# Kernel optimization log

Hardware: AMD Instinct MI355X
Metric: run time of the kernel (lower is better)

## Reference

```python
import jax, jax.numpy as jnp
import numpy as np
from jax import lax

C = 64      # mid_channels
CR = 16     # reduced channels (C // reduction_ratio 4)
G = 4       # groups (C // group_channels 16)
K = 7       # involution kernel size
L = 6       # number of involution layers (n_layers - 2)
EPS = 1e-5
DN = ('NCHW', 'OIHW', 'NCHW')


def conv3(x, w, b):
    # 3x3 conv, stride 1, no padding (torch Conv2d default)
    y = lax.conv_general_dilated(x, w, (1, 1), [(0, 0), (0, 0)], dimension_numbers=DN)
    return y + b[None, :, None, None]


def conv1x1(x, w, b):
    # pointwise conv as einsum over channels
    return jnp.einsum('oi,bihw->bohw', w, x) + b[None, :, None, None]


def involution(x, wr, br, g, bt, mu, var, ws, bs):
    B, Cc, H, W = x.shape
    # kernel generation: 1x1 reduce -> BN (eval) -> ReLU -> 1x1 span
    t = conv1x1(x, wr, br)
    t = (t - mu[None, :, None, None]) * (g * jax.lax.rsqrt(var + EPS))[None, :, None, None] + bt[None, :, None, None]
    t = jax.nn.relu(t)
    w = conv1x1(t, ws, bs)                    # (B, G*K*K, H, W)
    w = w.reshape(B, G, K * K, H, W)
    # unfold: patches ordered (C, Kh, Kw) along channel dim, matching torch unfold
    p = lax.conv_general_dilated_patches(x, (K, K), (1, 1), [(K // 2, K // 2)] * 2, dimension_numbers=DN)
    p = p.reshape(B, G, Cc // G, K * K, H, W)
    out = jnp.einsum('bgkhw,bgckhw->bgchw', w, p)
    return out.reshape(B, Cc, H, W)


def setup_inputs() -> dict:
    key = jax.random.key(0)
    ks = jax.random.split(key, 9)
    s = 0.05
    return {
        'input_tensor': jax.random.normal(ks[0], (1, 3, 128, 128), jnp.float32),
        'conv_in_w': jax.random.normal(ks[1], (C, 3, 3, 3), jnp.float32) * s,
        'conv_in_b': jax.random.normal(ks[2], (C,), jnp.float32) * s,
        'w_reduce': jax.random.normal(ks[3], (L, CR, C), jnp.float32) * s,
        'b_reduce': jax.random.normal(ks[4], (L, CR), jnp.float32) * s,
        'bn_gamma': jnp.ones((L, CR), jnp.float32),
        'bn_beta': jnp.zeros((L, CR), jnp.float32),
        'bn_mean': jnp.zeros((L, CR), jnp.float32),
        'bn_var': jnp.ones((L, CR), jnp.float32),
        'w_span': jax.random.normal(ks[5], (L, G * K * K, CR), jnp.float32) * s,
        'b_span': jax.random.normal(ks[6], (L, G * K * K), jnp.float32) * s,
        'conv_out_w': jax.random.normal(ks[7], (2 * C, C, 3, 3), jnp.float32) * s,
        'conv_out_b': jax.random.normal(ks[8], (2 * C,), jnp.float32) * s,
    }


def reference(input_tensor, conv_in_w, conv_in_b, w_reduce, b_reduce, bn_gamma,
              bn_beta, bn_mean, bn_var, w_span, b_span, conv_out_w, conv_out_b):
    x = conv3(input_tensor, conv_in_w, conv_in_b)          # (1, 64, 126, 126)
    for i in range(L):
        x = jax.nn.relu(involution(x, w_reduce[i], b_reduce[i], bn_gamma[i],
                                   bn_beta[i], bn_mean[i], bn_var[i],
                                   w_span[i], b_span[i]))
    return conv3(x, conv_out_w, conv_out_b)                # (1, 128, 124, 124)
```

## Files before the change

kernel.cpp:

```cpp
#include <hip/hip_runtime.h>

#define IH 126
#define IW 126
#define HW 15876
#define OH 124
#define OW 124
#define OHW 15376

__global__ __launch_bounds__(256) void conv_in_kernel(
    const float* __restrict__ x, const float* __restrict__ w,
    const float* __restrict__ b, float* __restrict__ y)
{
  int pix = blockIdx.x * 256 + threadIdx.x;
  if (pix >= HW) return;
  int oc = blockIdx.y;
  int h  = pix / IW;
  int wc = pix - h * IW;
  const float* wp = w + oc * 27;
  float acc = b[oc];
#pragma unroll
  for (int ci = 0; ci < 3; ci++)
#pragma unroll
    for (int ky = 0; ky < 3; ky++)
#pragma unroll
      for (int kx = 0; kx < 3; kx++)
        acc = fmaf(x[ci * 128 * 128 + (h + ky) * 128 + (wc + kx)],
                   wp[ci * 9 + ky * 3 + kx], acc);
  y[oc * HW + pix] = acc;
}

#define XSW(c, pos) ((c) ^ (((pos) & 7) << 3))
#define WVP 36
__global__ __launch_bounds__(512, 4) void inv_kernel(
    const float* __restrict__ x, float* __restrict__ y,
    const float* __restrict__ wr, const float* __restrict__ br,
    const float* __restrict__ gam, const float* __restrict__ bet,
    const float* __restrict__ mu, const float* __restrict__ var,
    const float* __restrict__ wspan, const float* __restrict__ bspan)
{
  __shared__ __align__(16) float xs[140][68];
  __shared__ __align__(16) float wvs[196 * WVP];
  __shared__ __align__(16) float tss[640];
  float* ob  = &xs[0][0];

  int tid = threadIdx.x;
  int bx = blockIdx.x & 15, by = blockIdx.x >> 4;
  int ox0 = bx * 8, oy0 = by * 4;
  int xh0 = ox0 - 3, yh0 = oy0 - 3;

  for (int idx = tid; idx < 140 * 64; idx += 512) {
    int c = idx / 140;
    int pos = idx - c * 140;
    int row = pos / 14;
    int col = pos - row * 14;
    int gy = yh0 + row, gx = xh0 + col;
    float v = 0.f;
    if (gy >= 0 && gy < IH && gx >= 0 && gx < IW)
      v = x[c * HW + gy * IW + gx];
    xs[pos][XSW(c, pos)] = v;
  }
  __syncthreads();

  int w_ = __builtin_amdgcn_readfirstlane(tid >> 6);
  int ln = tid & 63;
  int p  = ln & 31;
  int prow = p >> 3, pcol = p & 7;
  int pc = (prow + 3) * 14 + (pcol + 3);

  {
    int cr0 = 2 * w_;
    const float* wa = wr + cr0 * 64;
    const float* wb = wa + 64;
    float a0 = 0.f, a1 = 0.f;
    int xsw = (pc & 7) << 3;
#pragma unroll
    for (int ci = 0; ci < 64; ci += 4) {
      int cis = ci ^ xsw;
      float4 xv = *(const float4*)&xs[pc][cis];
      a0 = fmaf(xv.x, wa[cis + 0], a0); a1 = fmaf(xv.x, wb[cis + 0], a1);
      a0 = fmaf(xv.y, wa[cis + 1], a0); a1 = fmaf(xv.y, wb[cis + 1], a1);
      a0 = fmaf(xv.z, wa[cis + 2], a0); a1 = fmaf(xv.z, wb[cis + 2], a1);
      a0 = fmaf(xv.w, wa[cis + 3], a0); a1 = fmaf(xv.w, wb[cis + 3], a1);
    }
    float s0 = gam[cr0]     * rsqrtf(var[cr0]     + 1e-5f);
    float s1 = gam[cr0 + 1] * rsqrtf(var[cr0 + 1] + 1e-5f);
    float t0 = (a0 + br[cr0]     - mu[cr0])     * s0 + bet[cr0];
    float t1 = (a1 + br[cr0 + 1] - mu[cr0 + 1]) * s1 + bet[cr0 + 1];
    if (ln < 32) {
      tss[p * 20 + cr0]     = fmaxf(t0, 0.f);
      tss[p * 20 + cr0 + 1] = fmaxf(t1, 0.f);
    }
  }
  __syncthreads();

  {
    float tv[16];
#pragma unroll
    for (int i = 0; i < 4; i++) {
      float4 t4 = *(const float4*)&tss[p * 20 + 4 * i];
      tv[4 * i] = t4.x; tv[4 * i + 1] = t4.y;
      tv[4 * i + 2] = t4.z; tv[4 * i + 3] = t4.w;
    }
    for (int j = 0; j < 25; j++) {
      int pair = w_ + 8 * j;
      if (pair < 196) {
        const float* wk = wspan + pair * 16;
        float a = bspan[pair];
#pragma unroll
        for (int i = 0; i < 16; i++) a = fmaf(tv[i], wk[i], a);
        if (ln < 32) wvs[pair * WVP + pcol * 4 + prow] = a;
      }
    }
  }
  __syncthreads();

  float acc0 = 0.f, acc1 = 0.f, acc2 = 0.f, acc3 = 0.f;
  {
    int c = ln;
    int g = ln >> 4;
    float xw[4][7];
#pragma unroll
    for (int r = 0; r < 4; r++)
#pragma unroll
      for (int kx = 0; kx < 7; kx++) {
        int pos = r * 14 + w_ + kx;
        xw[r][kx] = xs[pos][XSW(c, pos)];
      }
#pragma unroll
    for (int ky = 0; ky < 7; ky++) {
      if (ky > 0) {
#pragma unroll
        for (int r = 0; r < 3; r++)
#pragma unroll
          for (int kx = 0; kx < 7; kx++) xw[r][kx] = xw[r + 1][kx];
#pragma unroll
        for (int kx = 0; kx < 7; kx++) {
          int pos = (ky + 3) * 14 + w_ + kx;
          xw[3][kx] = xs[pos][XSW(c, pos)];
        }
      }
#pragma unroll
      for (int kx = 0; kx < 7; kx++) {
        int k = ky * 7 + kx;
        float4 w4 = *(const float4*)&wvs[(g * 49 + k) * WVP + w_ * 4];
        acc0 = fmaf(w4.x, xw[0][kx], acc0);
        acc1 = fmaf(w4.y, xw[1][kx], acc1);
        acc2 = fmaf(w4.z, xw[2][kx], acc2);
        acc3 = fmaf(w4.w, xw[3][kx], acc3);
      }
    }
  }
  __syncthreads();

  {
    int c = ln;
    ob[c * 33 + 0 * 8 + w_] = fmaxf(acc0, 0.f);
    ob[c * 33 + 1 * 8 + w_] = fmaxf(acc1, 0.f);
    ob[c * 33 + 2 * 8 + w_] = fmaxf(acc2, 0.f);
    ob[c * 33 + 3 * 8 + w_] = fmaxf(acc3, 0.f);
  }
  __syncthreads();
  for (int j = tid; j < 2048; j += 512) {
    int c2 = j >> 5, pp = j & 31;
    int pr = pp >> 3, pc2 = pp & 7;
    int gy = oy0 + pr, gx = ox0 + pc2;
    if (gy < IH && gx < IW)
      y[c2 * HW + gy * IW + gx] = ob[c2 * 33 + pp];
  }
}

__global__ __launch_bounds__(256) void transpose_w_kernel(
    const float* __restrict__ w, float* __restrict__ wt)
{
  int i = blockIdx.x * 256 + threadIdx.x;
  if (i >= 128 * 64 * 9) return;
  int oc = i / 576;
  int rem = i - oc * 576;
  int ci = rem / 9;
  int k = rem - ci * 9;
  wt[(k * 64 + ci) * 128 + oc] = w[i];
}

__global__ __launch_bounds__(256, 6) void conv_out_kernel(
    const float* __restrict__ x, const float* __restrict__ wt,
    const float* __restrict__ b, float* __restrict__ y)
{
  __shared__ __align__(16) float xsm[16 * 100 * 4];
  int tid = threadIdx.x;
  int bx = blockIdx.x & 15, by = blockIdx.x >> 4;
  int oy0 = by * 8, ox0 = bx * 8;

  for (int u = tid; u < 1600; u += 256) {
    int cq = u / 100;
    int pos = u - cq * 100;
    int row = pos / 10;
    int col = pos - row * 10;
    int gy = oy0 + row, gx = ox0 + col;
    float4 v = make_float4(0.f, 0.f, 0.f, 0.f);
    if (gy < IH && gx < IW) {
      const float* xp = x + cq * 4 * HW + gy * IW + gx;
      v.x = xp[0]; v.y = xp[HW]; v.z = xp[2 * HW]; v.w = xp[3 * HW];
    }
    *(float4*)&xsm[u * 4] = v;
  }
  __syncthreads();

  int ln = tid & 63;
  int px = ln & 7, py = ln >> 3;
  int wv_ = __builtin_amdgcn_readfirstlane(tid >> 6);
  int oc8 = blockIdx.y * 32 + wv_ * 8;

  float acc[8];
#pragma unroll
  for (int j = 0; j < 8; j++) acc[j] = b[oc8 + j];

#pragma unroll
  for (int ky = 0; ky < 3; ky++) {
#pragma unroll
    for (int kx = 0; kx < 3; kx++) {
      int k = ky * 3 + kx;
      int pidx = (py + ky) * 10 + px + kx;
      const float* wp = wt + k * 64 * 128 + oc8;
#pragma unroll 4
      for (int cq = 0; cq < 16; cq++) {
        float4 xv = *(const float4*)&xsm[(cq * 100 + pidx) * 4];
        const float* wq = wp + cq * 4 * 128;
#pragma unroll
        for (int j = 0; j < 8; j++) {
          acc[j] = fmaf(xv.x, wq[0 * 128 + j], acc[j]);
          acc[j] = fmaf(xv.y, wq[1 * 128 + j], acc[j]);
          acc[j] = fmaf(xv.z, wq[2 * 128 + j], acc[j]);
          acc[j] = fmaf(xv.w, wq[3 * 128 + j], acc[j]);
        }
      }
    }
  }

  int oy = oy0 + py, ox = ox0 + px;
  if (oy < OH && ox < OW) {
#pragma unroll
    for (int j = 0; j < 8; j++)
      y[(oc8 + j) * OHW + oy * OW + ox] = acc[j];
  }
}

extern "C" void kernel_launch(void* const* d_in, const int* in_sizes, int n_in,
                              void* d_out, int out_size, void* d_ws, size_t ws_size,
                              hipStream_t stream)
{
  const float* input = (const float*)d_in[0];
  const float* ciw   = (const float*)d_in[1];
  const float* cib   = (const float*)d_in[2];
  const float* wred  = (const float*)d_in[3];
  const float* bred  = (const float*)d_in[4];
  const float* gam   = (const float*)d_in[5];
  const float* bet   = (const float*)d_in[6];
  const float* mu    = (const float*)d_in[7];
  const float* var   = (const float*)d_in[8];
  const float* wspan = (const float*)d_in[9];
  const float* bspan = (const float*)d_in[10];
  const float* cow   = (const float*)d_in[11];
  const float* cob   = (const float*)d_in[12];
  float* out = (float*)d_out;

  float* bufA = (float*)d_ws;
  float* bufB = bufA + (1 << 20);
  float* wt   = bufA + (1 << 21);

  transpose_w_kernel<<<288, 256, 0, stream>>>(cow, wt);
  conv_in_kernel<<<dim3(63, 64), 256, 0, stream>>>(input, ciw, cib, bufA);

  float* cur = bufA; float* nxt = bufB;
  for (int i = 0; i < 6; i++) {
    inv_kernel<<<512, 512, 0, stream>>>(cur, nxt,
        wred + i * 16 * 64, bred + i * 16, gam + i * 16, bet + i * 16,
        mu + i * 16, var + i * 16, wspan + i * 196 * 16, bspan + i * 196);
    float* t = cur; cur = nxt; nxt = t;
  }
  conv_out_kernel<<<dim3(256, 4), 256, 0, stream>>>(cur, wt, cob, out);
}
```

Before: 263.2 us.

## Fuse six involution layers into one cooperative kernel with grid sync

```diff
diff --git a/kernel.cpp b/kernel.cpp
--- a/kernel.cpp
+++ b/kernel.cpp
@@ -1,4 +1,7 @@
 #include <hip/hip_runtime.h>
+#include <hip/hip_cooperative_groups.h>
+
+namespace cg = cooperative_groups;
 
 #define IH 126
 #define IW 126
@@ -31,6 +34,163 @@
 
 #define XSW(c, pos) ((c) ^ (((pos) & 7) << 3))
 #define WVP 36
+
+__global__ __launch_bounds__(512, 4) void inv_all_kernel(
+    float* __restrict__ bufA, float* __restrict__ bufB,
+    const float* __restrict__ wr0, const float* __restrict__ br0,
+    const float* __restrict__ gam0, const float* __restrict__ bet0,
+    const float* __restrict__ mu0, const float* __restrict__ var0,
+    const float* __restrict__ wspan0, const float* __restrict__ bspan0)
+{
+  __shared__ __align__(16) float xs[140][68];
+  __shared__ __align__(16) float wvs[196 * WVP];
+  __shared__ __align__(16) float tss[640];
+  __shared__ __align__(16) float wsm[3136];
+  float* ob = &xs[0][0];
+
+  cg::grid_group grid = cg::this_grid();
+
+  int tid = threadIdx.x;
+  int bx = blockIdx.x & 15, by = blockIdx.x >> 4;
+  int ox0 = bx * 8, oy0 = by * 4;
+  int xh0 = ox0 - 3, yh0 = oy0 - 3;
+  int w_ = __builtin_amdgcn_readfirstlane(tid >> 6);
+  int ln = tid & 63;
+  int p  = ln & 31;
+  int prow = p >> 3, pcol = p & 7;
+  int pc = (prow + 3) * 14 + (pcol + 3);
+
+  for (int layer = 0; layer < 6; layer++) {
+    if (layer > 0) grid.sync();
+
+    const float* x     = (layer & 1) ? bufB : bufA;
+    float*       y     = (layer & 1) ? bufA : bufB;
+    const float* wr    = wr0    + layer * 16 * 64;
+    const float* br    = br0    + layer * 16;
+    const float* gam   = gam0   + layer * 16;
+    const float* bet   = bet0   + layer * 16;
+    const float* mu    = mu0    + layer * 16;
+    const float* var   = var0   + layer * 16;
+    const float* wspan = wspan0 + layer * 196 * 16;
+    const float* bspan = bspan0 + layer * 196;
+
+    for (int idx = tid; idx < 140 * 64; idx += 512) {
+      int c = idx / 140;
+      int pos = idx - c * 140;
+      int row = pos / 14;
+      int col = pos - row * 14;
+      int gy = yh0 + row, gx = xh0 + col;
+      float v = 0.f;
+      if (gy >= 0 && gy < IH && gx >= 0 && gx < IW)
+        v = x[c * HW + gy * IW + gx];
+      xs[pos][XSW(c, pos)] = v;
+    }
+    for (int j = tid; j < 3136; j += 512) wsm[j] = wspan[j];
+    __syncthreads();
+
+    {
+      int cr0 = 2 * w_;
+      const float* wa = wr + cr0 * 64;
+      const float* wb = wa + 64;
+      float a0 = 0.f, a1 = 0.f;
+      int xsw = (pc & 7) << 3;
+#pragma unroll
+      for (int ci = 0; ci < 64; ci += 4) {
+        int cis = ci ^ xsw;
+        float4 xv = *(const float4*)&xs[pc][cis];
+        a0 = fmaf(xv.x, wa[cis + 0], a0); a1 = fmaf(xv.x, wb[cis + 0], a1);
+        a0 = fmaf(xv.y, wa[cis + 1], a0); a1 = fmaf(xv.y, wb[cis + 1], a1);
+        a0 = fmaf(xv.z, wa[cis + 2], a0); a1 = fmaf(xv.z, wb[cis + 2], a1);
+        a0 = fmaf(xv.w, wa[cis + 3], a0); a1 = fmaf(xv.w, wb[cis + 3], a1);
+      }
+      float s0 = gam[cr0]     * rsqrtf(var[cr0]     + 1e-5f);
+      float s1 = gam[cr0 + 1] * rsqrtf(var[cr0 + 1] + 1e-5f);
+      float t0 = (a0 + br[cr0]     - mu[cr0])     * s0 + bet[cr0];
+      float t1 = (a1 + br[cr0 + 1] - mu[cr0 + 1]) * s1 + bet[cr0 + 1];
+      if (ln < 32) {
+        tss[p * 20 + cr0]     = fmaxf(t0, 0.f);
+        tss[p * 20 + cr0 + 1] = fmaxf(t1, 0.f);
+      }
+    }
+    __syncthreads();
+
+    {
+      float tv[16];
+#pragma unroll
+      for (int i = 0; i < 4; i++) {
+        float4 t4 = *(const float4*)&tss[p * 20 + 4 * i];
+        tv[4 * i] = t4.x; tv[4 * i + 1] = t4.y;
+        tv[4 * i + 2] = t4.z; tv[4 * i + 3] = t4.w;
+      }
+      for (int j = 0; j < 25; j++) {
+        int pair = w_ + 8 * j;
+        if (pair < 196) {
+          const float* wk = &wsm[pair * 16];
+          float a = bspan[pair];
+#pragma unroll
+          for (int i = 0; i < 16; i++) a = fmaf(tv[i], wk[i], a);
+          if (ln < 32) wvs[pair * WVP + pcol * 4 + prow] = a;
+        }
+      }
+    }
+    __syncthreads();
+
+    float acc0 = 0.f, acc1 = 0.f, acc2 = 0.f, acc3 = 0.f;
+    {
+      int c = ln;
+      int g = ln >> 4;
+      float xw[4][7];
+#pragma unroll
+      for (int r = 0; r < 4; r++)
+#pragma unroll
+        for (int kx = 0; kx < 7; kx++) {
+          int pos = r * 14 + w_ + kx;
+          xw[r][kx] = xs[pos][XSW(c, pos)];
+        }
+#pragma unroll
+      for (int ky = 0; ky < 7; ky++) {
+        if (ky > 0) {
+#pragma unroll
+          for (int r = 0; r < 3; r++)
+#pragma unroll
+            for (int kx = 0; kx < 7; kx++) xw[r][kx] = xw[r + 1][kx];
+#pragma unroll
+          for (int kx = 0; kx < 7; kx++) {
+            int pos = (ky + 3) * 14 + w_ + kx;
+            xw[3][kx] = xs[pos][XSW(c, pos)];
+          }
+        }
+#pragma unroll
+        for (int kx = 0; kx < 7; kx++) {
+          int k = ky * 7 + kx;
+          float4 w4 = *(const float4*)&wvs[(g * 49 + k) * WVP + w_ * 4];
+          acc0 = fmaf(w4.x, xw[0][kx], acc0);
+          acc1 = fmaf(w4.y, xw[1][kx], acc1);
+          acc2 = fmaf(w4.z, xw[2][kx], acc2);
+          acc3 = fmaf(w4.w, xw[3][kx], acc3);
+        }
+      }
+    }
+    __syncthreads();
+
+    {
+      int c = ln;
+      ob[c * 33 + 0 * 8 + w_] = fmaxf(acc0, 0.f);
+      ob[c * 33 + 1 * 8 + w_] = fmaxf(acc1, 0.f);
+      ob[c * 33 + 2 * 8 + w_] = fmaxf(acc2, 0.f);
+      ob[c * 33 + 3 * 8 + w_] = fmaxf(acc3, 0.f);
+    }
+    __syncthreads();
+    for (int j = tid; j < 2048; j += 512) {
+      int c2 = j >> 5, pp = j & 31;
+      int pr = pp >> 3, pc2 = pp & 7;
+      int gy = oy0 + pr, gx = ox0 + pc2;
+      if (gy < IH && gx < IW)
+        y[c2 * HW + gy * IW + gx] = ob[c2 * 33 + pp];
+    }
+  }
+}
+
 __global__ __launch_bounds__(512, 4) void inv_kernel(
     const float* __restrict__ x, float* __restrict__ y,
     const float* __restrict__ wr, const float* __restrict__ br,
@@ -270,12 +430,23 @@
   transpose_w_kernel<<<288, 256, 0, stream>>>(cow, wt);
   conv_in_kernel<<<dim3(63, 64), 256, 0, stream>>>(input, ciw, cib, bufA);
 
-  float* cur = bufA; float* nxt = bufB;
-  for (int i = 0; i < 6; i++) {
-    inv_kernel<<<512, 512, 0, stream>>>(cur, nxt,
-        wred + i * 16 * 64, bred + i * 16, gam + i * 16, bet + i * 16,
-        mu + i * 16, var + i * 16, wspan + i * 196 * 16, bspan + i * 196);
-    float* t = cur; cur = nxt; nxt = t;
-  }
-  conv_out_kernel<<<dim3(256, 4), 256, 0, stream>>>(cur, wt, cob, out);
-}
+  {
+    void* args[] = {&bufA, &bufB, (void*)&wred, (void*)&bred, (void*)&gam,
+                    (void*)&bet, (void*)&mu, (void*)&var, (void*)&wspan,
+                    (void*)&bspan};
+    hipError_t e = hipLaunchCooperativeKernel(
+        reinterpret_cast<void*>(inv_all_kernel), dim3(512), dim3(512),
+        args, 0, stream);
+    if (e != hipSuccess) {
+      float* cur = bufA; float* nxt = bufB;
+      for (int i = 0; i < 6; i++) {
+        inv_kernel<<<512, 512, 0, stream>>>(cur, nxt,
+            wred + i * 16 * 64, bred + i * 16, gam + i * 16, bet + i * 16,
+            mu + i * 16, var + i * 16, wspan + i * 196 * 16, bspan + i * 196);
+        float* t = cur; cur = nxt; nxt = t;
+      }
+    }
+  }
+
+  conv_out_kernel<<<dim3(256, 4), 256, 0, stream>>>(bufA, wt, cob, out);
+}
```

Measured after the change: 634.7 us. +141.2%, slower.

## Switch intermediate activations from channel-major to pixel-major (HWC) layout

Applied to the files above, without the earlier changes.

```diff
diff --git a/kernel.cpp b/kernel.cpp
--- a/kernel.cpp
+++ b/kernel.cpp
@@ -7,13 +7,16 @@
 #define OW 124
 #define OHW 15376
 
+
 __global__ __launch_bounds__(256) void conv_in_kernel(
     const float* __restrict__ x, const float* __restrict__ w,
     const float* __restrict__ b, float* __restrict__ y)
 {
-  int pix = blockIdx.x * 256 + threadIdx.x;
+  int tid = threadIdx.x;
+  int oc = tid & 63;
+  int w_ = __builtin_amdgcn_readfirstlane(tid >> 6);
+  int pix = blockIdx.x * 4 + w_;
   if (pix >= HW) return;
-  int oc = blockIdx.y;
   int h  = pix / IW;
   int wc = pix - h * IW;
   const float* wp = w + oc * 27;
@@ -26,11 +29,12 @@
       for (int kx = 0; kx < 3; kx++)
         acc = fmaf(x[ci * 128 * 128 + (h + ky) * 128 + (wc + kx)],
                    wp[ci * 9 + ky * 3 + kx], acc);
-  y[oc * HW + pix] = acc;
+  y[pix * 64 + oc] = acc;
 }
 
 #define XSW(c, pos) ((c) ^ (((pos) & 7) << 3))
 #define WVP 36
+
 __global__ __launch_bounds__(512, 4) void inv_kernel(
     const float* __restrict__ x, float* __restrict__ y,
     const float* __restrict__ wr, const float* __restrict__ br,
@@ -41,23 +45,22 @@
   __shared__ __align__(16) float xs[140][68];
   __shared__ __align__(16) float wvs[196 * WVP];
   __shared__ __align__(16) float tss[640];
-  float* ob  = &xs[0][0];
 
   int tid = threadIdx.x;
   int bx = blockIdx.x & 15, by = blockIdx.x >> 4;
   int ox0 = bx * 8, oy0 = by * 4;
   int xh0 = ox0 - 3, yh0 = oy0 - 3;
 
-  for (int idx = tid; idx < 140 * 64; idx += 512) {
-    int c = idx / 140;
-    int pos = idx - c * 140;
+  for (int idx = tid; idx < 140 * 16; idx += 512) {
+    int pos = idx >> 4;
+    int c4  = (idx & 15) << 2;
     int row = pos / 14;
     int col = pos - row * 14;
     int gy = yh0 + row, gx = xh0 + col;
-    float v = 0.f;
+    float4 v = make_float4(0.f, 0.f, 0.f, 0.f);
     if (gy >= 0 && gy < IH && gx >= 0 && gx < IW)
-      v = x[c * HW + gy * IW + gx];
-    xs[pos][XSW(c, pos)] = v;
+      v = *(const float4*)&x[(gy * IW + gx) * 64 + c4];
+    *(float4*)&xs[pos][XSW(c4, pos)] = v;
   }
   __syncthreads();
 
@@ -150,22 +153,17 @@
       }
     }
   }
-  __syncthreads();
 
   {
     int c = ln;
-    ob[c * 33 + 0 * 8 + w_] = fmaxf(acc0, 0.f);
-    ob[c * 33 + 1 * 8 + w_] = fmaxf(acc1, 0.f);
-    ob[c * 33 + 2 * 8 + w_] = fmaxf(acc2, 0.f);
-    ob[c * 33 + 3 * 8 + w_] = fmaxf(acc3, 0.f);
-  }
-  __syncthreads();
-  for (int j = tid; j < 2048; j += 512) {
-    int c2 = j >> 5, pp = j & 31;
-    int pr = pp >> 3, pc2 = pp & 7;
-    int gy = oy0 + pr, gx = ox0 + pc2;
-    if (gy < IH && gx < IW)
-      y[c2 * HW + gy * IW + gx] = ob[c2 * 33 + pp];
+    int gx = ox0 + w_;
+    if (gx < IW) {
+      int base = (oy0 * IW + gx) * 64 + c;
+      y[base]               = fmaxf(acc0, 0.f);
+      y[base + 1 * IW * 64] = fmaxf(acc1, 0.f);
+      if (oy0 + 2 < IH) y[base + 2 * IW * 64] = fmaxf(acc2, 0.f);
+      if (oy0 + 3 < IH) y[base + 3 * IW * 64] = fmaxf(acc3, 0.f);
+    }
   }
 }
 
@@ -197,10 +195,8 @@
     int col = pos - row * 10;
     int gy = oy0 + row, gx = ox0 + col;
     float4 v = make_float4(0.f, 0.f, 0.f, 0.f);
-    if (gy < IH && gx < IW) {
-      const float* xp = x + cq * 4 * HW + gy * IW + gx;
-      v.x = xp[0]; v.y = xp[HW]; v.z = xp[2 * HW]; v.w = xp[3 * HW];
-    }
+    if (gy < IH && gx < IW)
+      v = *(const float4*)&x[(gy * IW + gx) * 64 + cq * 4];
     *(float4*)&xsm[u * 4] = v;
   }
   __syncthreads();
@@ -268,7 +264,7 @@
   float* wt   = bufA + (1 << 21);
 
   transpose_w_kernel<<<288, 256, 0, stream>>>(cow, wt);
-  conv_in_kernel<<<dim3(63, 64), 256, 0, stream>>>(input, ciw, cib, bufA);
+  conv_in_kernel<<<3969, 256, 0, stream>>>(input, ciw, cib, bufA);
 
   float* cur = bufA; float* nxt = bufB;
   for (int i = 0; i < 6; i++) {
```

New measurement: 238.1 us. -9.5%, faster.
